# Optimization experiments

Measured on AMD Instinct MI355X. Metric: run time of the kernel, lower is better.

## Reference

```python
import jax, jax.numpy as jnp
import numpy as np

B, S, DIMS, HEAD = 4, 4096, 1024, 16
HD = DIMS // HEAD


def setup_inputs() -> dict:
    key = jax.random.key(0)
    ks = jax.random.split(key, 9)
    inv = 1.0 / np.sqrt(DIMS)
    return {
        "x": jax.random.normal(ks[0], (B, S, DIMS), dtype=jnp.float32),
        "Wq": jax.random.normal(ks[1], (DIMS, DIMS), dtype=jnp.float32) * inv,
        "bq": jax.random.normal(ks[2], (DIMS,), dtype=jnp.float32) * 0.02,
        "Wk": jax.random.normal(ks[3], (DIMS, DIMS), dtype=jnp.float32) * inv,
        "bk": jax.random.normal(ks[4], (DIMS,), dtype=jnp.float32) * 0.02,
        "Wv": jax.random.normal(ks[5], (DIMS, DIMS), dtype=jnp.float32) * inv,
        "bv": jax.random.normal(ks[6], (DIMS,), dtype=jnp.float32) * 0.02,
        "Wo": jax.random.normal(ks[7], (DIMS, DIMS), dtype=jnp.float32) * inv,
        "bo": jax.random.normal(ks[8], (DIMS,), dtype=jnp.float32) * 0.02,
        "skip_pattern": 4,
    }


def reference(x, Wq, bq, Wk, bk, Wv, bv, Wo, bo, skip_pattern):
    b, s, _ = x.shape
    scale = DIMS ** (-0.5)  # NOTE: source scales by full dims, not head_dim

    def proj(W, bias):
        # torch Linear: x @ W.T + b ; then [B,S,H,HD] -> [B,H,S,HD]
        y = jnp.einsum('bsd,ed->bse', x, W) + bias
        return y.reshape(b, s, HEAD, HD).transpose(0, 2, 1, 3)

    q = proj(Wq, bq)
    k = proj(Wk, bk)
    v = proj(Wv, bv)

    # strided KV downsample (static python-int stride -> static shapes under jit)
    k_s = k[:, :, ::skip_pattern, :]  # [B,H,S//skip,HD]
    v_s = v[:, :, ::skip_pattern, :]

    scores = jnp.einsum('bhqd,bhkd->bhqk', q, k_s) * scale
    attn = jax.nn.softmax(scores, axis=-1)
    out = jnp.einsum('bhqk,bhkd->bhqd', attn, v_s)  # [B,H,S,HD]
    out = out.transpose(0, 2, 1, 3).reshape(b, s, DIMS)
    return jnp.einsum('bsd,ed->bse', out, Wo) + bo
```

## Files before the change

### kernel.cpp

```cpp
#include <hip/hip_runtime.h>
#include <hip/hip_bf16.h>
#include <stdint.h>


using short8 = short __attribute__((ext_vector_type(8)));
using f32x4  = float __attribute__((ext_vector_type(4)));
using f32x16 = float __attribute__((ext_vector_type(16)));

#define MFMA16(A,B,C) __builtin_amdgcn_mfma_f32_16x16x32_bf16((A),(B),(C),0,0,0)
#define MFMA32(A,B,C) __builtin_amdgcn_mfma_f32_32x32x16_bf16((A),(B),(C),0,0,0)

#define QSC 0.0450842200277800f

#define VT_OFF 4194304

__device__ __forceinline__ unsigned short f2bf(float f) {
  unsigned int x = __float_as_uint(f);
  x += 0x7fffu + ((x >> 16) & 1u);
  return (unsigned short)(x >> 16);
}

__device__ __forceinline__ unsigned pack2(float a, float b) {
  float2 t; t.x = a; t.y = b;
  union { __hip_bfloat162 h; unsigned u; } cv;
  cv.h = __float22bfloat162_rn(t);
  return cv.u;
}

__device__ __forceinline__ float fexp2(float x) {
  float r; asm("v_exp_f32 %0, %1" : "=v"(r) : "v"(x)); return r;
}

#define PLSWAP(a,b) asm volatile("v_permlane32_swap_b32 %0, %1" : "+v"(a), "+v"(b))

__device__ __forceinline__ void gld_lds16(const void* g, void* l) {
  __builtin_amdgcn_global_load_lds(
      (const __attribute__((address_space(1))) void*)g,
      (__attribute__((address_space(3))) void*)l,
      16, 0, 0);
}

__device__ __forceinline__ void wait_vm8_barrier() {
  __builtin_amdgcn_sched_barrier(0);
  asm volatile("s_waitcnt vmcnt(8)" ::: "memory");
  __builtin_amdgcn_s_barrier();
  __builtin_amdgcn_sched_barrier(0);
}
__device__ __forceinline__ void wait_vm0_barrier() {
  __builtin_amdgcn_sched_barrier(0);
  asm volatile("s_waitcnt vmcnt(0)" ::: "memory");
  __builtin_amdgcn_s_barrier();
  __builtin_amdgcn_sched_barrier(0);
}
__device__ __forceinline__ void wait_lgkm_barrier() {
  __builtin_amdgcn_sched_barrier(0);
  asm volatile("s_waitcnt lgkmcnt(0)" ::: "memory");
  __builtin_amdgcn_s_barrier();
  __builtin_amdgcn_sched_barrier(0);
}

__global__ __launch_bounds__(256) void cvtall_kernel(
    const float* __restrict__ x,  unsigned short* __restrict__ xb,
    const float* __restrict__ w0, const float* __restrict__ w1,
    const float* __restrict__ w2, const float* __restrict__ w3,
    unsigned short* __restrict__ o0, unsigned short* __restrict__ o1,
    unsigned short* __restrict__ o2, unsigned short* __restrict__ o3) {
  int bid = blockIdx.x, tid = threadIdx.x;
  const float* in; unsigned short* out; int n4, i0, stride;
  if (bid < 2048) {
    in = x; out = xb; n4 = 4194304; i0 = bid * 256 + tid; stride = 2048 * 256;
  } else {
    int t = (bid - 2048) >> 7;
    switch (t) {
      case 0: in = w0; out = o0; break;
      case 1: in = w1; out = o1; break;
      case 2: in = w2; out = o2; break;
      default: in = w3; out = o3; break;
    }
    n4 = 262144; i0 = ((bid - 2048) & 127) * 256 + tid; stride = 128 * 256;
  }
  for (int i = i0; i < n4; i += stride) {
    float4 v = ((const float4*)in)[i];
    ushort4 o;
    o.x = f2bf(v.x); o.y = f2bf(v.y); o.z = f2bf(v.z); o.w = f2bf(v.w);
    ((ushort4*)out)[i] = o;
  }
}

template<int MODE, int ROWMUL>
__device__ __forceinline__ void gemm_body(
    unsigned short* __restrict__ lA, unsigned short* __restrict__ lB,
    const unsigned short* __restrict__ A,
    const unsigned short* __restrict__ W,
    const float* __restrict__ biasA,
    const float* __restrict__ biasB,
    void* __restrict__ outp,
    int NB, int bid, int nwg)
{
  constexpr int K = 1024;
  int vid = (bid & 7) * (nwg >> 3) + (bid >> 3);
  int bm = vid / NB, bn = vid % NB;

  int tid = threadIdx.x;
  int w = tid >> 6, l = tid & 63;
  int wm = w >> 1, wn = w & 1;
  int fr = l & 15, fk = l >> 4;

  int sr = w * 16 + (l >> 2);
  int sc = ((l & 3) ^ ((l >> 3) & 3)) * 8;
  const unsigned short* ga0 = A + (size_t)ROWMUL * (size_t)(bm * 128 + sr) * K + sc;
  const unsigned short* ga1 = A + (size_t)ROWMUL * (size_t)(bm * 128 + 64 + sr) * K + sc;
  const unsigned short* gb0 = W + (size_t)(bn * 128 + sr) * K + sc;
  const unsigned short* gb1 = W + (size_t)(bn * 128 + 64 + sr) * K + sc;
  int la0 = (w * 16) * 32;
  int la1 = (64 + w * 16) * 32;

  int physk = (fk ^ ((fr >> 1) & 3)) * 8;

  f32x4 acc[4][4];
  #pragma unroll
  for (int i = 0; i < 4; ++i)
    #pragma unroll
    for (int j = 0; j < 4; ++j) acc[i][j] = (f32x4){0.f, 0.f, 0.f, 0.f};

#define GSTAGE(BUF, KT)                                                         \
  {                                                                             \
    int o = (BUF) * 8192;                                                       \
    gld_lds16(ga0 + (KT) * 64,      &lA[o + la0]);                              \
    gld_lds16(ga0 + (KT) * 64 + 32, &lA[o + la0 + 4096]);                       \
    gld_lds16(ga1 + (KT) * 64,      &lA[o + la1]);                              \
    gld_lds16(ga1 + (KT) * 64 + 32, &lA[o + la1 + 4096]);                       \
    gld_lds16(gb0 + (KT) * 64,      &lB[o + la0]);                              \
    gld_lds16(gb0 + (KT) * 64 + 32, &lB[o + la0 + 4096]);                       \
    gld_lds16(gb1 + (KT) * 64,      &lB[o + la1]);                              \
    gld_lds16(gb1 + (KT) * 64 + 32, &lB[o + la1 + 4096]);                       \
  }

  GSTAGE(0, 0);

  for (int kt = 0; kt < K / 64; ++kt) {
    int b = kt & 1;
    if (kt + 1 < K / 64) {
      GSTAGE(b ^ 1, kt + 1);
      wait_vm8_barrier();
    } else {
      wait_vm0_barrier();
    }

    #pragma unroll
    for (int kh = 0; kh < 2; ++kh) {
      int base = b * 8192 + kh * 4096;
      short8 af[4], bf[4];
      #pragma unroll
      for (int mi = 0; mi < 4; ++mi)
        af[mi] = *(const short8*)&lA[base + (wm * 64 + mi * 16 + fr) * 32 + physk];
      #pragma unroll
      for (int nj = 0; nj < 4; ++nj)
        bf[nj] = *(const short8*)&lB[base + (wn * 64 + nj * 16 + fr) * 32 + physk];
      __builtin_amdgcn_s_setprio(1);
      #pragma unroll
      for (int mi = 0; mi < 4; ++mi)
        #pragma unroll
        for (int nj = 0; nj < 4; ++nj)
          acc[mi][nj] = MFMA16(af[mi], bf[nj], acc[mi][nj]);
      __builtin_amdgcn_s_setprio(0);
    }

    wait_lgkm_barrier();
  }
#undef GSTAGE

  float bv[4];
  #pragma unroll
  for (int nj = 0; nj < 4; ++nj) {
    int n = bn * 128 + wn * 64 + nj * 16 + fr;
    bv[nj] = (MODE == 4) ? (n < 1024 ? biasA[n] : biasB[n - 1024]) : biasA[n];
  }

  #pragma unroll
  for (int mi = 0; mi < 4; ++mi) {
    #pragma unroll
    for (int nj = 0; nj < 4; ++nj) {
      #pragma unroll
      for (int j = 0; j < 4; ++j) {
        int m = bm * 128 + wm * 64 + mi * 16 + fk * 4 + j;
        int n = bn * 128 + wn * 64 + nj * 16 + fr;
        float v = acc[mi][nj][j] + bv[nj];
        if (MODE == 0) {
          ((float*)outp)[(size_t)m * 1024 + n] = v;
        } else if (MODE == 1) {
          size_t idx = (size_t)((m >> 12) * 16 + (n >> 6)) * 262144
                     + (size_t)(m & 4095) * 64 + (n & 63);
          ((unsigned short*)outp)[idx] = f2bf(v * QSC);
        } else {
          if (n < 1024) {
            size_t idx = (size_t)((m >> 10) * 16 + (n >> 6)) * 65536
                       + (size_t)(m & 1023) * 64 + (n & 63);
            ((unsigned short*)outp)[idx] = f2bf(v);
          } else {
            int nn = n - 1024;
            size_t idx = (size_t)VT_OFF
                       + (size_t)((m >> 10) * 16 + (nn >> 6)) * 65536
                       + (size_t)(nn & 63) * 1024 + (m & 1023);
            ((unsigned short*)outp)[idx] = f2bf(v);
          }
        }
      }
    }
  }
}

__global__ __launch_bounds__(256) void proj_fused_kernel(
    const unsigned short* __restrict__ xb,
    const unsigned short* __restrict__ wqb,
    const unsigned short* __restrict__ wkb,
    const float* __restrict__ bq,
    const float* __restrict__ bk,
    const float* __restrict__ bv,
    unsigned short* __restrict__ qb,
    unsigned short* __restrict__ kb)
{
  __shared__ unsigned short lA[2 * 8192];
  __shared__ unsigned short lB[2 * 8192];
  int bid = blockIdx.x;
  if (bid < 1024) {
    gemm_body<1, 1>(lA, lB, xb, wqb, bq, bq, qb, 8, bid, 1024);
  } else {
    gemm_body<4, 4>(lA, lB, xb, wkb, bk, bv, kb, 16, bid - 1024, 512);
  }
}

__global__ __launch_bounds__(256) void oproj_kernel(
    const unsigned short* __restrict__ ab,
    const unsigned short* __restrict__ wob,
    const float* __restrict__ bo,
    float* __restrict__ out)
{
  __shared__ unsigned short lA[2 * 8192];
  __shared__ unsigned short lB[2 * 8192];
  gemm_body<0, 1>(lA, lB, ab, wob, bo, bo, out, 8, blockIdx.x, 1024);
}

__global__ __launch_bounds__(512) void attn_kernel(
    const unsigned short* __restrict__ Q,
    const unsigned short* __restrict__ Ks,
    const unsigned short* __restrict__ Vt,
    unsigned short* __restrict__ O)
{
  __shared__ unsigned short lds[16384];
  unsigned short* lsK = lds;
  unsigned short* lsV = lds + 8192;

  int bid = blockIdx.x;
  int vid = (bid & 7) * 128 + (bid >> 3);
  int bh = vid >> 4;
  int qt = vid & 15;
  int tid = threadIdx.x;
  int w = tid >> 6, l = tid & 63;
  int l31 = l & 31, hi = l >> 5;
  int q0 = qt * 256 + w * 32;

  short8 qf[4];
  {
    const unsigned short* qp = Q + ((size_t)bh * 4096 + q0 + l31) * 64 + hi * 8;
    #pragma unroll
    for (int s = 0; s < 4; ++s) qf[s] = *(const short8*)(qp + s * 16);
  }

  const unsigned short* Kbh = Ks + (size_t)bh * 65536;
  const unsigned short* Vbh = Vt + (size_t)bh * 65536;

  int r = w * 8 + (l >> 3);
  int c0 = ((l & 7) ^ (l >> 3)) * 8;
  int dst = w * 512;

#define STAGE(BUF, KC)                                                          \
  {                                                                             \
    const unsigned short* Kb = Kbh + (KC) * 4096;                               \
    const unsigned short* Vb = Vbh + (KC) * 64;                                 \
    gld_lds16(Kb + r * 64 + c0, &lsK[(BUF) * 4096 + dst]);                      \
    gld_lds16(Vb + (size_t)r * 1024 + c0, &lsV[(BUF) * 4096 + dst]);            \
  }

  float lrun = 0.f;
  f32x16 oa0, oa1;
  #pragma unroll
  for (int rr = 0; rr < 16; ++rr) { oa0[rr] = 0.f; oa1[rr] = 0.f; }

  STAGE(0, 0);
  __syncthreads();

  int rb0 = l31 * 64, rb1 = rb0 + 2048;
  int rsw = l31 & 7;

  for (int kc = 0; kc < 16; ++kc) {
    int b = kc & 1;
    if (kc + 1 < 16) STAGE(b ^ 1, kc + 1);

    const unsigned short* Kl = &lsK[b * 4096];
    const unsigned short* Vl = &lsV[b * 4096];

    f32x16 s0, s1;
    #pragma unroll
    for (int rr = 0; rr < 16; ++rr) { s0[rr] = 0.f; s1[rr] = 0.f; }
    __builtin_amdgcn_s_setprio(1);
    #pragma unroll
    for (int s = 0; s < 4; ++s) {
      int co = ((hi + 2 * s) ^ rsw) * 8;
      short8 kf0 = *(const short8*)&Kl[rb0 + co];
      short8 kf1 = *(const short8*)&Kl[rb1 + co];
      s0 = MFMA32(kf0, qf[s], s0);
      s1 = MFMA32(kf1, qf[s], s1);
    }
    __builtin_amdgcn_s_setprio(0);

    unsigned pk0[8], pk1[8];
    float sm0 = 0.f, sm1 = 0.f, sm2 = 0.f, sm3 = 0.f;
    #pragma unroll
    for (int i = 0; i < 4; ++i) {
      float a = fexp2(s0[2*i]), bb = fexp2(s0[2*i+1]);
      sm0 += a + bb; pk0[i] = pack2(a, bb);
    }
    #pragma unroll
    for (int i = 4; i < 8; ++i) {
      float a = fexp2(s0[2*i]), bb = fexp2(s0[2*i+1]);
      sm1 += a + bb; pk0[i] = pack2(a, bb);
    }
    #pragma unroll
    for (int i = 0; i < 4; ++i) {
      float a = fexp2(s1[2*i]), bb = fexp2(s1[2*i+1]);
      sm2 += a + bb; pk1[i] = pack2(a, bb);
    }
    #pragma unroll
    for (int i = 4; i < 8; ++i) {
      float a = fexp2(s1[2*i]), bb = fexp2(s1[2*i+1]);
      sm3 += a + bb; pk1[i] = pack2(a, bb);
    }
    lrun += (sm0 + sm1) + (sm2 + sm3);

    short8 pf[4];
    #pragma unroll
    for (int half = 0; half < 2; ++half) {
      #pragma unroll
      for (int sl = 0; sl < 2; ++sl) {
        unsigned a0 = half ? pk1[sl*4+0] : pk0[sl*4+0];
        unsigned a1 = half ? pk1[sl*4+1] : pk0[sl*4+1];
        unsigned b0 = half ? pk1[sl*4+2] : pk0[sl*4+2];
        unsigned b1 = half ? pk1[sl*4+3] : pk0[sl*4+3];
        unsigned t0 = a0; PLSWAP(t0, b0);
        unsigned t1 = a1; PLSWAP(t1, b1);
        union { unsigned u[4]; short8 s8; } u;
        u.u[0] = t0;
        u.u[1] = t1;
        u.u[2] = b0;
        u.u[3] = b1;
        pf[half * 2 + sl] = u.s8;
      }
    }

    __builtin_amdgcn_s_setprio(1);
    #pragma unroll
    for (int s = 0; s < 4; ++s) {
      int co = ((hi + 2 * s) ^ rsw) * 8;
      short8 vf0 = *(const short8*)&Vl[rb0 + co];
      short8 vf1 = *(const short8*)&Vl[rb1 + co];
      oa0 = MFMA32(vf0, pf[s], oa0);
      oa1 = MFMA32(vf1, pf[s], oa1);
    }
    __builtin_amdgcn_s_setprio(0);

    __syncthreads();
  }
#undef STAGE

  lrun += __shfl_xor(lrun, 32);
  float inv = 1.0f / lrun;

  unsigned short* ob = lds + w * 2048;
  #pragma unroll
  for (int dblk = 0; dblk < 2; ++dblk) {
    #pragma unroll
    for (int rr = 0; rr < 16; ++rr) {
      float v = (dblk ? oa1[rr] : oa0[rr]) * inv;
      int d = dblk * 32 + (rr & 3) + 8 * (rr >> 2) + 4 * hi;
      ob[l31 * 64 + (d ^ ((l31 & 7) << 3))] = f2bf(v);
    }
  }
  int b = bh >> 4, h = bh & 15;
  #pragma unroll
  for (int pass = 0; pass < 8; ++pass) {
    int qq = pass * 4 + (l >> 4);
    int cc = (l & 15) * 4;
    ushort4 vv = *(const ushort4*)&ob[qq * 64 + (cc ^ ((qq & 7) << 3))];
    *(ushort4*)&O[((size_t)b * 4096 + q0 + qq) * 1024 + h * 64 + cc] = vv;
  }
}

extern "C" void kernel_launch(void* const* d_in, const int* in_sizes, int n_in,
                              void* d_out, int out_size, void* d_ws, size_t ws_size,
                              hipStream_t stream) {
  const float* x  = (const float*)d_in[0];
  const float* Wq = (const float*)d_in[1];
  const float* bq = (const float*)d_in[2];
  const float* Wk = (const float*)d_in[3];
  const float* bk = (const float*)d_in[4];
  const float* Wv = (const float*)d_in[5];
  const float* bv = (const float*)d_in[6];
  const float* Wo = (const float*)d_in[7];
  const float* bo = (const float*)d_in[8];
  float* out = (float*)d_out;

  unsigned short* ws  = (unsigned short*)d_ws;
  unsigned short* xb  = ws;
  unsigned short* wqb = xb  + 16777216;
  unsigned short* wkb = wqb + 1048576;
  unsigned short* wvb = wkb + 1048576;
  unsigned short* wob = wvb + 1048576;
  unsigned short* qb  = wob + 1048576;
  unsigned short* kb  = qb  + 16777216;
  unsigned short* vtb = kb  + 4194304;
  unsigned short* ab  = vtb + 4194304;

  cvtall_kernel<<<2560, 256, 0, stream>>>(x, xb, Wq, Wk, Wv, Wo, wqb, wkb, wvb, wob);
  proj_fused_kernel<<<1536, 256, 0, stream>>>(xb, wqb, wkb, bq, bk, bv, qb, kb);
  attn_kernel<<<1024, 512, 0, stream>>>(qb, kb, vtb, ab);
  oproj_kernel<<<1024, 256, 0, stream>>>(ab, wob, bo, out);
}
```

Baseline: 222.8 us.

## Use 256x128 GEMM tiles with 8 waves and phased interleaved prefetch

The projection and output GEMMs now use 256x128 block tiles computed by 512 threads, with K-steps of 64 held in a single swizzled LDS row. Global-to-LDS prefetch of the next tile is spread across four MFMA phases separated by barriers, so loads interleave with compute. The aim is more reuse of each B tile and better overlap of memory with MFMA work. In exchange, LDS use grows, there are more barriers per iteration, and fewer blocks are launched, which may lower occupancy and wave balance.

```diff
diff --git a/kernel.cpp b/kernel.cpp
--- a/kernel.cpp
+++ b/kernel.cpp
@@ -11,7 +11,6 @@
 #define MFMA32(A,B,C) __builtin_amdgcn_mfma_f32_32x32x16_bf16((A),(B),(C),0,0,0)
 
 #define QSC 0.0450842200277800f
-
 #define VT_OFF 4194304
 
 __device__ __forceinline__ unsigned short f2bf(float f) {
@@ -40,9 +39,9 @@
       16, 0, 0);
 }
 
-__device__ __forceinline__ void wait_vm8_barrier() {
-  __builtin_amdgcn_sched_barrier(0);
-  asm volatile("s_waitcnt vmcnt(8)" ::: "memory");
+__device__ __forceinline__ void wait_vm2_barrier() {
+  __builtin_amdgcn_sched_barrier(0);
+  asm volatile("s_waitcnt vmcnt(2)" ::: "memory");
   __builtin_amdgcn_s_barrier();
   __builtin_amdgcn_sched_barrier(0);
 }
@@ -55,6 +54,11 @@
 __device__ __forceinline__ void wait_lgkm_barrier() {
   __builtin_amdgcn_sched_barrier(0);
   asm volatile("s_waitcnt lgkmcnt(0)" ::: "memory");
+  __builtin_amdgcn_s_barrier();
+  __builtin_amdgcn_sched_barrier(0);
+}
+__device__ __forceinline__ void phase_barrier() {
+  __builtin_amdgcn_sched_barrier(0);
   __builtin_amdgcn_s_barrier();
   __builtin_amdgcn_sched_barrier(0);
 }
@@ -88,7 +92,7 @@
 }
 
 template<int MODE, int ROWMUL>
-__device__ __forceinline__ void gemm_body(
+__device__ __forceinline__ void gemm_body256(
     unsigned short* __restrict__ lA, unsigned short* __restrict__ lB,
     const unsigned short* __restrict__ A,
     const unsigned short* __restrict__ W,
@@ -106,16 +110,16 @@
   int wm = w >> 1, wn = w & 1;
   int fr = l & 15, fk = l >> 4;
 
-  int sr = w * 16 + (l >> 2);
-  int sc = ((l & 3) ^ ((l >> 3) & 3)) * 8;
-  const unsigned short* ga0 = A + (size_t)ROWMUL * (size_t)(bm * 128 + sr) * K + sc;
-  const unsigned short* ga1 = A + (size_t)ROWMUL * (size_t)(bm * 128 + 64 + sr) * K + sc;
-  const unsigned short* gb0 = W + (size_t)(bn * 128 + sr) * K + sc;
-  const unsigned short* gb1 = W + (size_t)(bn * 128 + 64 + sr) * K + sc;
-  int la0 = (w * 16) * 32;
-  int la1 = (64 + w * 16) * 32;
-
-  int physk = (fk ^ ((fr >> 1) & 3)) * 8;
+  int srow = w * 8 + (l >> 3);
+  int pcs = ((l & 7) ^ (l >> 3)) * 8;
+  const unsigned short* gA = A + (size_t)ROWMUL * ((size_t)(bm * 256 + srow) * K) + pcs;
+  const unsigned short* gB = W + (size_t)(bn * 128 + srow) * K + pcs;
+  int ldst = w * 512;
+
+#define ST_A(B_, KT, I) gld_lds16(gA + (size_t)ROWMUL * 64 * (I) * K + (KT) * 64, \
+                                  &lA[(B_) * 16384 + (I) * 4096 + ldst])
+#define ST_B(B_, KT, I) gld_lds16(gB + (size_t)64 * (I) * K + (KT) * 64, \
+                                  &lB[(B_) * 8192 + (I) * 4096 + ldst])
 
   f32x4 acc[4][4];
   #pragma unroll
@@ -123,52 +127,56 @@
     #pragma unroll
     for (int j = 0; j < 4; ++j) acc[i][j] = (f32x4){0.f, 0.f, 0.f, 0.f};
 
-#define GSTAGE(BUF, KT)                                                         \
-  {                                                                             \
-    int o = (BUF) * 8192;                                                       \
-    gld_lds16(ga0 + (KT) * 64,      &lA[o + la0]);                              \
-    gld_lds16(ga0 + (KT) * 64 + 32, &lA[o + la0 + 4096]);                       \
-    gld_lds16(ga1 + (KT) * 64,      &lA[o + la1]);                              \
-    gld_lds16(ga1 + (KT) * 64 + 32, &lA[o + la1 + 4096]);                       \
-    gld_lds16(gb0 + (KT) * 64,      &lB[o + la0]);                              \
-    gld_lds16(gb0 + (KT) * 64 + 32, &lB[o + la0 + 4096]);                       \
-    gld_lds16(gb1 + (KT) * 64,      &lB[o + la1]);                              \
-    gld_lds16(gb1 + (KT) * 64 + 32, &lB[o + la1 + 4096]);                       \
-  }
-
-  GSTAGE(0, 0);
-
-  for (int kt = 0; kt < K / 64; ++kt) {
+  int rxor = fr & 7;
+
+  ST_A(0, 0, 0); ST_A(0, 0, 1); ST_A(0, 0, 2); ST_A(0, 0, 3);
+  ST_B(0, 0, 0); ST_B(0, 0, 1);
+
+  for (int kt = 0; kt < 16; ++kt) {
     int b = kt & 1;
-    if (kt + 1 < K / 64) {
-      GSTAGE(b ^ 1, kt + 1);
-      wait_vm8_barrier();
-    } else {
-      wait_vm0_barrier();
-    }
-
-    #pragma unroll
-    for (int kh = 0; kh < 2; ++kh) {
-      int base = b * 8192 + kh * 4096;
-      short8 af[4], bf[4];
+    int abA = b * 16384, abB = b * 8192;
+    bool pre = (kt + 1 < 16);
+
+#define PHASE(MI)                                                               \
+    {                                                                           \
+      short8 af[2];                                                             \
+      _Pragma("unroll")                                                         \
+      for (int kh = 0; kh < 2; ++kh)                                            \
+        af[kh] = *(const short8*)&lA[abA + (wm * 64 + (MI) * 16 + fr) * 64      \
+                                     + (((kh * 4 + fk) ^ rxor) * 8)];           \
+      __builtin_amdgcn_s_setprio(1);                                            \
+      _Pragma("unroll")                                                         \
+      for (int nj = 0; nj < 4; ++nj)                                            \
+        _Pragma("unroll")                                                       \
+        for (int kh = 0; kh < 2; ++kh)                                          \
+          acc[MI][nj] = MFMA16(af[kh], bfr[nj][kh], acc[MI][nj]);               \
+      __builtin_amdgcn_s_setprio(0);                                            \
+    }
+
+    if (pre) { ST_A(b ^ 1, kt + 1, 0); ST_A(b ^ 1, kt + 1, 1); }
+    if (pre) wait_vm2_barrier(); else wait_vm0_barrier();
+    short8 bfr[4][2];
+    #pragma unroll
+    for (int nj = 0; nj < 4; ++nj)
       #pragma unroll
-      for (int mi = 0; mi < 4; ++mi)
-        af[mi] = *(const short8*)&lA[base + (wm * 64 + mi * 16 + fr) * 32 + physk];
-      #pragma unroll
-      for (int nj = 0; nj < 4; ++nj)
-        bf[nj] = *(const short8*)&lB[base + (wn * 64 + nj * 16 + fr) * 32 + physk];
-      __builtin_amdgcn_s_setprio(1);
-      #pragma unroll
-      for (int mi = 0; mi < 4; ++mi)
-        #pragma unroll
-        for (int nj = 0; nj < 4; ++nj)
-          acc[mi][nj] = MFMA16(af[mi], bf[nj], acc[mi][nj]);
-      __builtin_amdgcn_s_setprio(0);
-    }
-
+      for (int kh = 0; kh < 2; ++kh)
+        bfr[nj][kh] = *(const short8*)&lB[abB + (wn * 64 + nj * 16 + fr) * 64
+                                         + (((kh * 4 + fk) ^ rxor) * 8)];
+    PHASE(0);
+    phase_barrier();
+    if (pre) { ST_A(b ^ 1, kt + 1, 2); ST_A(b ^ 1, kt + 1, 3); }
+    PHASE(1);
+    phase_barrier();
+    if (pre) { ST_B(b ^ 1, kt + 1, 0); }
+    PHASE(2);
+    phase_barrier();
+    if (pre) { ST_B(b ^ 1, kt + 1, 1); }
+    PHASE(3);
     wait_lgkm_barrier();
-  }
-#undef GSTAGE
+#undef PHASE
+  }
+#undef ST_A
+#undef ST_B
 
   float bv[4];
   #pragma unroll
@@ -183,7 +191,7 @@
     for (int nj = 0; nj < 4; ++nj) {
       #pragma unroll
       for (int j = 0; j < 4; ++j) {
-        int m = bm * 128 + wm * 64 + mi * 16 + fk * 4 + j;
+        int m = bm * 256 + wm * 64 + mi * 16 + fk * 4 + j;
         int n = bn * 128 + wn * 64 + nj * 16 + fr;
         float v = acc[mi][nj][j] + bv[nj];
         if (MODE == 0) {
@@ -210,7 +218,7 @@
   }
 }
 
-__global__ __launch_bounds__(256) void proj_fused_kernel(
+__global__ __launch_bounds__(512) void proj_fused_kernel(
     const unsigned short* __restrict__ xb,
     const unsigned short* __restrict__ wqb,
     const unsigned short* __restrict__ wkb,
@@ -220,25 +228,25 @@
     unsigned short* __restrict__ qb,
     unsigned short* __restrict__ kb)
 {
-  __shared__ unsigned short lA[2 * 8192];
+  __shared__ unsigned short lA[2 * 16384];
   __shared__ unsigned short lB[2 * 8192];
   int bid = blockIdx.x;
-  if (bid < 1024) {
-    gemm_body<1, 1>(lA, lB, xb, wqb, bq, bq, qb, 8, bid, 1024);
+  if (bid < 512) {
+    gemm_body256<1, 1>(lA, lB, xb, wqb, bq, bq, qb, 8, bid, 512);
   } else {
-    gemm_body<4, 4>(lA, lB, xb, wkb, bk, bv, kb, 16, bid - 1024, 512);
-  }
-}
-
-__global__ __launch_bounds__(256) void oproj_kernel(
+    gemm_body256<4, 4>(lA, lB, xb, wkb, bk, bv, kb, 16, bid - 512, 256);
+  }
+}
+
+__global__ __launch_bounds__(512) void oproj_kernel(
     const unsigned short* __restrict__ ab,
     const unsigned short* __restrict__ wob,
     const float* __restrict__ bo,
     float* __restrict__ out)
 {
-  __shared__ unsigned short lA[2 * 8192];
+  __shared__ unsigned short lA[2 * 16384];
   __shared__ unsigned short lB[2 * 8192];
-  gemm_body<0, 1>(lA, lB, ab, wob, bo, bo, out, 8, blockIdx.x, 1024);
+  gemm_body256<0, 1>(lA, lB, ab, wob, bo, bo, out, 8, blockIdx.x, 512);
 }
 
 __global__ __launch_bounds__(512) void attn_kernel(
@@ -422,7 +430,7 @@
   unsigned short* ab  = vtb + 4194304;
 
   cvtall_kernel<<<2560, 256, 0, stream>>>(x, xb, Wq, Wk, Wv, Wo, wqb, wkb, wvb, wob);
-  proj_fused_kernel<<<1536, 256, 0, stream>>>(xb, wqb, wkb, bq, bk, bv, qb, kb);
+  proj_fused_kernel<<<768, 512, 0, stream>>>(xb, wqb, wkb, bq, bk, bv, qb, kb);
   attn_kernel<<<1024, 512, 0, stream>>>(qb, kb, vtb, ab);
-  oproj_kernel<<<1024, 256, 0, stream>>>(ab, wob, bo, out);
-}
+  oproj_kernel<<<512, 512, 0, stream>>>(ab, wob, bo, out);
+}
```

New measurement: 296.5 us. 1.33x slower.
